# Performance work log

Hardware: AMD Instinct MI355X
Metric: run time of the kernel (lower is better)

Reference implementation:

```python
import jax, jax.numpy as jnp
import numpy as np

B, N, F, H, O = 8, 256, 128, 128, 64

def setup_inputs() -> dict:
    key = jax.random.key(0)
    ks = jax.random.split(key, 16)
    s = 0.02
    return {
        "local_x": jax.random.normal(ks[0], (B, N, F), jnp.float32),
        "global_x": jax.random.normal(ks[1], (B, N, F), jnp.float32),
        "mask": jax.random.uniform(ks[2], (B, N, N), jnp.float32),
        "key_idx": jax.random.randint(ks[3], (B,), 0, N),
        "hidden_state": jax.random.normal(ks[4], (B, N, H), jnp.float32),
        "fc_w": jax.random.normal(ks[5], (H, 3 * F), jnp.float32) * s,
        "fc_b": jnp.zeros((H,), jnp.float32),
        "ln_g": jnp.ones((H,), jnp.float32),
        "ln_b": jnp.zeros((H,), jnp.float32),
        "w_ih": jax.random.normal(ks[6], (3 * H, H), jnp.float32) * s,
        "w_hh": jax.random.normal(ks[7], (3 * H, H), jnp.float32) * s,
        "b_ih": jnp.zeros((3 * H,), jnp.float32),
        "b_hh": jnp.zeros((3 * H,), jnp.float32),
        "out_w": jax.random.normal(ks[8], (O, H), jnp.float32) * s,
        "out_b": jnp.zeros((O,), jnp.float32),
    }

def _forward(local_x, global_x, mask, key_idx, hidden_state,
             fc_w, fc_b, ln_g, ln_b, w_ih, w_hh, b_ih, b_hh, out_w, out_b):
    b, n, f = local_x.shape
    # masked mean aggregation over agents: same math as expand*mask then sum/den
    denom = mask.sum(axis=2, keepdims=True) + 1e-6            # [B,N,1]
    weak = jnp.einsum('bij,bjf->bif', mask, global_x) / denom  # [B,N,F]
    key_feat = jnp.take_along_axis(global_x, key_idx[:, None, None], axis=1)  # [B,1,F]
    key_feat = jnp.broadcast_to(key_feat, (b, n, f))
    combined = jnp.concatenate([local_x, weak, key_feat], axis=-1)  # [B,N,3F]
    h = combined @ fc_w.T + fc_b
    mu = h.mean(-1, keepdims=True)
    var = ((h - mu) ** 2).mean(-1, keepdims=True)
    h = (h - mu) / jnp.sqrt(var + 1e-5) * ln_g + ln_b
    x = jax.nn.relu(h)
    xf = x.reshape(-1, H)
    hf = hidden_state.reshape(-1, H)
    gi = xf @ w_ih.T + b_ih   # [BN,3H]
    gh = hf @ w_hh.T + b_hh
    i_r, i_z, i_n = jnp.split(gi, 3, axis=-1)
    h_r, h_z, h_n = jnp.split(gh, 3, axis=-1)
    r = jax.nn.sigmoid(i_r + h_r)
    z = jax.nn.sigmoid(i_z + h_z)
    nn_ = jnp.tanh(i_n + r * h_n)
    h_new = (1.0 - z) * nn_ + z * hf
    out = h_new @ out_w.T + out_b
    return out.reshape(b, n, -1), h_new.reshape(b, n, -1)

def reference(local_x, global_x, mask, key_idx, hidden_state,
              fc_w, fc_b, ln_g, ln_b, w_ih, w_hh, b_ih, b_hh, out_w, out_b):
    return _forward(local_x, global_x, mask, key_idx, hidden_state,
                    fc_w, fc_b, ln_g, ln_b, w_ih, w_hh, b_ih, b_hh, out_w, out_b)
```

## Files before the change

kernel.cpp:

```cpp
#include <hip/hip_runtime.h>

namespace {

typedef unsigned short ushort_t;
typedef unsigned int uint_t;
typedef __attribute__((ext_vector_type(8))) short short8v;
typedef __attribute__((ext_vector_type(4))) float f32x4;

constexpr int kB = 8, kN = 256, kF = 128, kH = 128, kO = 64;
constexpr int kR = 8;
constexpr int kTPB = 1024;
constexpr int kOut0 = kB * kN * kO;

constexpr int FW_WHH  = 0;
constexpr int FW_FCW  = 96;
constexpr int FW_WIH  = 192;
constexpr int FW_OUTW = 288;
constexpr int FW_GX   = 304;
constexpr int FW_TOTAL = 816;

union Frag {
    uint_t  u[4];
    short8v v;
};

__device__ __forceinline__ float waveReduceAdd(float v) {
    v += __shfl_xor(v, 1);
    v += __shfl_xor(v, 2);
    v += __shfl_xor(v, 4);
    v += __shfl_xor(v, 8);
    v += __shfl_xor(v, 16);
    v += __shfl_xor(v, 32);
    return v;
}

__device__ __forceinline__ ushort_t cvt1(float f) {
    return (ushort_t)((__float_as_uint(f) + 0x8000u) >> 16);
}
__device__ __forceinline__ uint_t pk(float f0, float f1) {
    uint_t b0 = __float_as_uint(f0) + 0x8000u;
    uint_t b1 = __float_as_uint(f1) + 0x8000u;
    return (b1 & 0xFFFF0000u) | (b0 >> 16);
}
__device__ __forceinline__ float b2f(ushort_t h) {
    return __uint_as_float(((uint_t)h) << 16);
}
__device__ __forceinline__ void loadWFrag(const float* __restrict__ p, Frag& b) {
    float4 lo = *(const float4*)p;
    float4 hi = *(const float4*)(p + 4);
    b.u[0] = pk(lo.x, lo.y);
    b.u[1] = pk(lo.z, lo.w);
    b.u[2] = pk(hi.x, hi.y);
    b.u[3] = pk(hi.z, hi.w);
}

__global__ __launch_bounds__(256) void convert_frags(
    const float* __restrict__ gx, const float* __restrict__ fc_w,
    const float* __restrict__ w_ih, const float* __restrict__ w_hh,
    const float* __restrict__ out_w, uint4* __restrict__ ws)
{
    const int gw = (int)((blockIdx.x * 256 + threadIdx.x) >> 6);
    if (gw >= FW_TOTAL) return;
    const int lane = threadIdx.x & 63;
    const int arow = lane & 15;
    const int kgrp = (lane >> 4) * 8;
    Frag fr;
    if (gw < FW_FCW) {
        int idx = gw - FW_WHH, t = idx >> 2, kf = idx & 3;
        loadWFrag(w_hh + (size_t)(t * 16 + arow) * kH + kf * 32 + kgrp, fr);
    } else if (gw < FW_WIH) {
        int idx = gw - FW_FCW, t = idx / 12, kf = idx % 12;
        loadWFrag(fc_w + (size_t)(t * 16 + arow) * 384 + kf * 32 + kgrp, fr);
    } else if (gw < FW_OUTW) {
        int idx = gw - FW_WIH, t = idx >> 2, kf = idx & 3;
        loadWFrag(w_ih + (size_t)(t * 16 + arow) * kH + kf * 32 + kgrp, fr);
    } else if (gw < FW_GX) {
        int idx = gw - FW_OUTW, t = idx >> 2, kf = idx & 3;
        loadWFrag(out_w + (size_t)(t * 16 + arow) * kH + kf * 32 + kgrp, fr);
    } else {
        int idx = gw - FW_GX;
        int bb = idx >> 6, rem = idx & 63, t = rem >> 3, kf = rem & 7;
        int k0 = kf * 32 + kgrp;
        const float* gp = gx + ((size_t)bb * kN + k0) * kF + t * 16 + arow;
        fr.u[0] = pk(gp[0 * kF], gp[1 * kF]);
        fr.u[1] = pk(gp[2 * kF], gp[3 * kF]);
        fr.u[2] = pk(gp[4 * kF], gp[5 * kF]);
        fr.u[3] = pk(gp[6 * kF], gp[7 * kF]);
    }
    ws[(size_t)gw * 64 + lane] = *(uint4*)fr.u;
}

__global__ __launch_bounds__(kTPB, 4) void weak_tie_fused(
    const float* __restrict__ lx, const float* __restrict__ gx,
    const float* __restrict__ mask, const int* __restrict__ key_idx,
    const float* __restrict__ hstate,
    const float* __restrict__ fc_b,
    const float* __restrict__ ln_g, const float* __restrict__ ln_b,
    const float* __restrict__ b_ih, const float* __restrict__ b_hh,
    const float* __restrict__ out_b,
    const uint4* __restrict__ ws,
    float* __restrict__ out)
{
    __shared__ __align__(16) ushort_t maskb[16][264];
    __shared__ __align__(16) ushort_t cmb[16][392];
    __shared__ __align__(16) ushort_t hf16[16][136];
    __shared__ __align__(16) ushort_t xb16[16][136];
    __shared__ __align__(16) ushort_t hnb16[16][136];
    __shared__ __align__(16) float hf32[kR * kH];
    __shared__ __align__(16) float hb[kR * kH];
    __shared__ __align__(16) ushort_t ghb[kR][384];
    __shared__ __align__(16) ushort_t gib[kR][384];
    __shared__ float denomInv[kR];

    const int tid  = threadIdx.x;
    const int b    = blockIdx.x >> 5;
    const int row0 = (blockIdx.x & 31) * kR;
    const int lane = tid & 63;
    const int wv   = tid >> 6;
    const int arow = lane & 15;
    const int kgrp = (lane >> 4) * 8;

    {
        const int r = tid >> 7, c = tid & 127;
        const float* mrow = mask + ((size_t)b * kN + row0) * kN;
        maskb[r][c]       = cvt1(mrow[r * 256 + c]);
        maskb[r][c + 128] = cvt1(mrow[r * 256 + c + 128]);
        const float* lrow = lx + ((size_t)b * kN + row0) * kF;
        cmb[r][c] = cvt1(lrow[tid]);
        const int ki = key_idx[b];
        cmb[r][256 + c] = cvt1(gx[((size_t)b * kN + ki) * kF + c]);
        const float* hrow = hstate + ((size_t)b * kN + row0) * kH;
        float hv = hrow[tid];
        hf32[tid] = hv;
        hf16[r][c] = cvt1(hv);
        uint_t* z;
        z = (uint_t*)&maskb[8][0]; for (int i = tid; i < 8 * 264 / 2; i += kTPB) z[i] = 0;
        z = (uint_t*)&cmb[8][0];   for (int i = tid; i < 8 * 392 / 2; i += kTPB) z[i] = 0;
        z = (uint_t*)&hf16[8][0];  for (int i = tid; i < 8 * 136 / 2; i += kTPB) z[i] = 0;
        z = (uint_t*)&xb16[8][0];  for (int i = tid; i < 8 * 136 / 2; i += kTPB) z[i] = 0;
        z = (uint_t*)&hnb16[8][0]; for (int i = tid; i < 8 * 136 / 2; i += kTPB) z[i] = 0;
    }
    __syncthreads();

    if (wv < 8) {
        int r = wv;
        float s = b2f(maskb[r][lane])       + b2f(maskb[r][lane + 64]) +
                  b2f(maskb[r][lane + 128]) + b2f(maskb[r][lane + 192]);
        s = waveReduceAdd(s);
        if (lane == 0) denomInv[r] = 1.0f / (s + 1e-6f);
    }
    __syncthreads();

    if (wv < 8) {
        const uint4* wsf = ws + ((size_t)(FW_GX + b * 64 + wv * 8) * 64 + lane);
        f32x4 acc = {0.f, 0.f, 0.f, 0.f};
        #pragma unroll
        for (int kf = 0; kf < 8; ++kf) {
            Frag a, bb;
            *(uint4*)a.u  = *(const uint4*)&maskb[arow][kf * 32 + kgrp];
            *(uint4*)bb.u = wsf[(size_t)kf * 64];
            acc = __builtin_amdgcn_mfma_f32_16x16x32_bf16(a.v, bb.v, acc, 0, 0, 0);
        }
        const int n0 = 16 * wv;
        #pragma unroll
        for (int j = 0; j < 4; ++j) {
            int row = (lane >> 4) * 4 + j;
            if (row < 8)
                cmb[row][128 + n0 + arow] = cvt1(acc[j] * denomInv[row]);
        }
    } else {
        const int w2 = wv - 8;
        Frag af[4];
        #pragma unroll
        for (int kf = 0; kf < 4; ++kf)
            *(uint4*)af[kf].u = *(const uint4*)&hf16[arow][kf * 32 + kgrp];
        #pragma unroll
        for (int t = 0; t < 3; ++t) {
            const int tile = w2 * 3 + t;
            const uint4* wsf = ws + ((size_t)(FW_WHH + tile * 4) * 64 + lane);
            f32x4 acc = {0.f, 0.f, 0.f, 0.f};
            #pragma unroll
            for (int kf = 0; kf < 4; ++kf) {
                Frag bb;
                *(uint4*)bb.u = wsf[(size_t)kf * 64];
                acc = __builtin_amdgcn_mfma_f32_16x16x32_bf16(af[kf].v, bb.v, acc, 0, 0, 0);
            }
            const int n0 = 16 * tile;
            #pragma unroll
            for (int j = 0; j < 4; ++j) {
                int row = (lane >> 4) * 4 + j;
                if (row < 8) ghb[row][n0 + arow] = cvt1(acc[j]);
            }
        }
    }
    __syncthreads();

    Frag bfr[12];
    if (wv < 8) {
        const uint4* wsf = ws + ((size_t)(FW_FCW + wv * 12) * 64 + lane);
        f32x4 acc = {0.f, 0.f, 0.f, 0.f};
        #pragma unroll
        for (int kf = 0; kf < 12; ++kf) {
            Frag a, bb;
            *(uint4*)a.u  = *(const uint4*)&cmb[arow][kf * 32 + kgrp];
            *(uint4*)bb.u = wsf[(size_t)kf * 64];
            acc = __builtin_amdgcn_mfma_f32_16x16x32_bf16(a.v, bb.v, acc, 0, 0, 0);
        }
        const int n0 = 16 * wv;
        #pragma unroll
        for (int j = 0; j < 4; ++j) {
            int row = (lane >> 4) * 4 + j;
            if (row < 8) hb[row * 128 + n0 + arow] = acc[j];
        }
    } else {
        const int w2 = wv - 8;
        #pragma unroll
        for (int t = 0; t < 3; ++t) {
            const int tile = w2 * 3 + t;
            const uint4* wsf = ws + ((size_t)(FW_WIH + tile * 4) * 64 + lane);
            #pragma unroll
            for (int kf = 0; kf < 4; ++kf)
                *(uint4*)bfr[t * 4 + kf].u = wsf[(size_t)kf * 64];
        }
    }
    __syncthreads();

    if (wv < 8) {
        int r = wv;
        float v0 = hb[r * 128 + lane]      + fc_b[lane];
        float v1 = hb[r * 128 + lane + 64] + fc_b[lane + 64];
        float s  = waveReduceAdd(v0 + v1);
        float ss = waveReduceAdd(v0 * v0 + v1 * v1);
        float mu   = s * (1.0f / 128.0f);
        float var  = ss * (1.0f / 128.0f) - mu * mu;
        float rstd = rsqrtf(var + 1e-5f);
        float x0 = fmaxf((v0 - mu) * rstd * ln_g[lane] + ln_b[lane], 0.f);
        float x1 = fmaxf((v1 - mu) * rstd * ln_g[lane + 64] + ln_b[lane + 64], 0.f);
        xb16[r][lane]      = cvt1(x0);
        xb16[r][lane + 64] = cvt1(x1);
    }
    __syncthreads();

    Frag obf[4];
    if (wv >= 8) {
        const int w2 = wv - 8;
        Frag af[4];
        #pragma unroll
        for (int kf = 0; kf < 4; ++kf)
            *(uint4*)af[kf].u = *(const uint4*)&xb16[arow][kf * 32 + kgrp];
        #pragma unroll
        for (int t = 0; t < 3; ++t) {
            const int n0 = 16 * (w2 * 3 + t);
            f32x4 acc = {0.f, 0.f, 0.f, 0.f};
            #pragma unroll
            for (int kf = 0; kf < 4; ++kf)
                acc = __builtin_amdgcn_mfma_f32_16x16x32_bf16(af[kf].v, bfr[t * 4 + kf].v, acc, 0, 0, 0);
            #pragma unroll
            for (int j = 0; j < 4; ++j) {
                int row = (lane >> 4) * 4 + j;
                if (row < 8) gib[row][n0 + arow] = cvt1(acc[j]);
            }
        }
    } else if (wv < 4) {
        const uint4* wsf = ws + ((size_t)(FW_OUTW + wv * 4) * 64 + lane);
        #pragma unroll
        for (int kf = 0; kf < 4; ++kf)
            *(uint4*)obf[kf].u = wsf[(size_t)kf * 64];
    }
    __syncthreads();

    {
        const int r = tid >> 7, fcol = tid & 127;
        float ir  = b2f(gib[r][fcol])       + b_ih[fcol];
        float iz  = b2f(gib[r][128 + fcol]) + b_ih[128 + fcol];
        float inn = b2f(gib[r][256 + fcol]) + b_ih[256 + fcol];
        float hr  = b2f(ghb[r][fcol])       + b_hh[fcol];
        float hz  = b2f(ghb[r][128 + fcol]) + b_hh[128 + fcol];
        float hn  = b2f(ghb[r][256 + fcol]) + b_hh[256 + fcol];
        float rg = 1.0f / (1.0f + __expf(-(ir + hr)));
        float zg = 1.0f / (1.0f + __expf(-(iz + hz)));
        float ng = tanhf(inn + rg * hn);
        float hprev = hf32[r * 128 + fcol];
        float hnew = (1.0f - zg) * ng + zg * hprev;
        hnb16[r][fcol] = cvt1(hnew);
        out[kOut0 + ((size_t)(b * kN + row0 + r)) * kH + fcol] = hnew;
    }
    __syncthreads();

    if (wv < 4) {
        const int n0 = 16 * wv;
        Frag af[4];
        #pragma unroll
        for (int kf = 0; kf < 4; ++kf)
            *(uint4*)af[kf].u = *(const uint4*)&hnb16[arow][kf * 32 + kgrp];
        f32x4 acc = {0.f, 0.f, 0.f, 0.f};
        #pragma unroll
        for (int kf = 0; kf < 4; ++kf)
            acc = __builtin_amdgcn_mfma_f32_16x16x32_bf16(af[kf].v, obf[kf].v, acc, 0, 0, 0);
        float ob = out_b[n0 + arow];
        #pragma unroll
        for (int j = 0; j < 4; ++j) {
            int row = (lane >> 4) * 4 + j;
            if (row < 8)
                out[((size_t)(b * kN + row0 + row)) * kO + n0 + arow] = acc[j] + ob;
        }
    }
}

}

extern "C" void kernel_launch(void* const* d_in, const int* in_sizes, int n_in,
                              void* d_out, int out_size, void* d_ws, size_t ws_size,
                              hipStream_t stream) {
    const float* lx      = (const float*)d_in[0];
    const float* gx      = (const float*)d_in[1];
    const float* mask    = (const float*)d_in[2];
    const int*   key_idx = (const int*)  d_in[3];
    const float* hs      = (const float*)d_in[4];
    const float* fc_w    = (const float*)d_in[5];
    const float* fc_b    = (const float*)d_in[6];
    const float* ln_g    = (const float*)d_in[7];
    const float* ln_b    = (const float*)d_in[8];
    const float* w_ih    = (const float*)d_in[9];
    const float* w_hh    = (const float*)d_in[10];
    const float* b_ih    = (const float*)d_in[11];
    const float* b_hh    = (const float*)d_in[12];
    const float* out_w   = (const float*)d_in[13];
    const float* out_b   = (const float*)d_in[14];
    float* out = (float*)d_out;
    uint4* ws = (uint4*)d_ws;

    hipLaunchKernelGGL(convert_frags, dim3((FW_TOTAL * 64) / 256), dim3(256), 0, stream,
                       gx, fc_w, w_ih, w_hh, out_w, ws);

    dim3 grid(kB * kN / kR);
    dim3 block(kTPB);
    hipLaunchKernelGGL(weak_tie_fused, grid, block, 0, stream,
                       lx, gx, mask, key_idx, hs,
                       fc_b, ln_g, ln_b,
                       b_ih, b_hh, out_b,
                       (const uint4*)ws, out);
}
```

Baseline: 19.32 us.

## Halve rows per block and rebalance waves across twice as many blocks

Each block now handles 4 node rows with 512 threads instead of 8 rows with 1024, doubling the grid to 512 blocks. The waves are reassigned: 4 waves each cover two output tiles of the aggregation and fc GEMMs, and 4 waves each cover six gate tiles. The zero-fill of the padding rows of the shared MFMA operand tiles is removed, since only rows 0-3 of each 16-row tile are written back. The aim is to spread the work over more CUs and shorten each block's serial critical path, at the cost of re-reading every weight fragment per block and wasting more of each 16-row MFMA tile.

```diff
diff --git a/kernel.cpp b/kernel.cpp
--- a/kernel.cpp
+++ b/kernel.cpp
@@ -8,8 +8,8 @@
 typedef __attribute__((ext_vector_type(4))) float f32x4;
 
 constexpr int kB = 8, kN = 256, kF = 128, kH = 128, kO = 64;
-constexpr int kR = 8;
-constexpr int kTPB = 1024;
+constexpr int kR = 4;
+constexpr int kTPB = 512;
 constexpr int kOut0 = kB * kN * kO;
 
 constexpr int FW_WHH  = 0;
@@ -113,8 +113,8 @@
     __shared__ float denomInv[kR];
 
     const int tid  = threadIdx.x;
-    const int b    = blockIdx.x >> 5;
-    const int row0 = (blockIdx.x & 31) * kR;
+    const int b    = blockIdx.x >> 6;
+    const int row0 = (blockIdx.x & 63) * kR;
     const int lane = tid & 63;
     const int wv   = tid >> 6;
     const int arow = lane & 15;
@@ -133,16 +133,10 @@
         float hv = hrow[tid];
         hf32[tid] = hv;
         hf16[r][c] = cvt1(hv);
-        uint_t* z;
-        z = (uint_t*)&maskb[8][0]; for (int i = tid; i < 8 * 264 / 2; i += kTPB) z[i] = 0;
-        z = (uint_t*)&cmb[8][0];   for (int i = tid; i < 8 * 392 / 2; i += kTPB) z[i] = 0;
-        z = (uint_t*)&hf16[8][0];  for (int i = tid; i < 8 * 136 / 2; i += kTPB) z[i] = 0;
-        z = (uint_t*)&xb16[8][0];  for (int i = tid; i < 8 * 136 / 2; i += kTPB) z[i] = 0;
-        z = (uint_t*)&hnb16[8][0]; for (int i = tid; i < 8 * 136 / 2; i += kTPB) z[i] = 0;
-    }
-    __syncthreads();
-
-    if (wv < 8) {
+    }
+    __syncthreads();
+
+    if (wv < kR) {
         int r = wv;
         float s = b2f(maskb[r][lane])       + b2f(maskb[r][lane + 64]) +
                   b2f(maskb[r][lane + 128]) + b2f(maskb[r][lane + 192]);
@@ -151,32 +145,37 @@
     }
     __syncthreads();
 
-    if (wv < 8) {
-        const uint4* wsf = ws + ((size_t)(FW_GX + b * 64 + wv * 8) * 64 + lane);
-        f32x4 acc = {0.f, 0.f, 0.f, 0.f};
-        #pragma unroll
-        for (int kf = 0; kf < 8; ++kf) {
-            Frag a, bb;
-            *(uint4*)a.u  = *(const uint4*)&maskb[arow][kf * 32 + kgrp];
-            *(uint4*)bb.u = wsf[(size_t)kf * 64];
-            acc = __builtin_amdgcn_mfma_f32_16x16x32_bf16(a.v, bb.v, acc, 0, 0, 0);
-        }
-        const int n0 = 16 * wv;
-        #pragma unroll
-        for (int j = 0; j < 4; ++j) {
-            int row = (lane >> 4) * 4 + j;
-            if (row < 8)
-                cmb[row][128 + n0 + arow] = cvt1(acc[j] * denomInv[row]);
+    if (wv < 4) {
+        Frag am[8];
+        #pragma unroll
+        for (int kf = 0; kf < 8; ++kf)
+            *(uint4*)am[kf].u = *(const uint4*)&maskb[arow][kf * 32 + kgrp];
+        #pragma unroll
+        for (int tt = 0; tt < 2; ++tt) {
+            const int t = wv * 2 + tt;
+            const uint4* wsf = ws + ((size_t)(FW_GX + b * 64 + t * 8) * 64 + lane);
+            f32x4 acc = {0.f, 0.f, 0.f, 0.f};
+            #pragma unroll
+            for (int kf = 0; kf < 8; ++kf) {
+                Frag bb;
+                *(uint4*)bb.u = wsf[(size_t)kf * 64];
+                acc = __builtin_amdgcn_mfma_f32_16x16x32_bf16(am[kf].v, bb.v, acc, 0, 0, 0);
+            }
+            const int n0 = 16 * t;
+            if ((lane >> 4) == 0) {
+                #pragma unroll
+                for (int j = 0; j < 4; ++j)
+                    cmb[j][128 + n0 + arow] = cvt1(acc[j] * denomInv[j]);
+            }
         }
     } else {
-        const int w2 = wv - 8;
         Frag af[4];
         #pragma unroll
         for (int kf = 0; kf < 4; ++kf)
             *(uint4*)af[kf].u = *(const uint4*)&hf16[arow][kf * 32 + kgrp];
         #pragma unroll
-        for (int t = 0; t < 3; ++t) {
-            const int tile = w2 * 3 + t;
+        for (int t6 = 0; t6 < 6; ++t6) {
+            const int tile = (wv - 4) * 6 + t6;
             const uint4* wsf = ws + ((size_t)(FW_WHH + tile * 4) * 64 + lane);
             f32x4 acc = {0.f, 0.f, 0.f, 0.f};
             #pragma unroll
@@ -186,46 +185,52 @@
                 acc = __builtin_amdgcn_mfma_f32_16x16x32_bf16(af[kf].v, bb.v, acc, 0, 0, 0);
             }
             const int n0 = 16 * tile;
-            #pragma unroll
-            for (int j = 0; j < 4; ++j) {
-                int row = (lane >> 4) * 4 + j;
-                if (row < 8) ghb[row][n0 + arow] = cvt1(acc[j]);
+            if ((lane >> 4) == 0) {
+                #pragma unroll
+                for (int j = 0; j < 4; ++j)
+                    ghb[j][n0 + arow] = cvt1(acc[j]);
             }
         }
     }
     __syncthreads();
 
     Frag bfr[12];
-    if (wv < 8) {
-        const uint4* wsf = ws + ((size_t)(FW_FCW + wv * 12) * 64 + lane);
-        f32x4 acc = {0.f, 0.f, 0.f, 0.f};
-        #pragma unroll
-        for (int kf = 0; kf < 12; ++kf) {
-            Frag a, bb;
-            *(uint4*)a.u  = *(const uint4*)&cmb[arow][kf * 32 + kgrp];
-            *(uint4*)bb.u = wsf[(size_t)kf * 64];
-            acc = __builtin_amdgcn_mfma_f32_16x16x32_bf16(a.v, bb.v, acc, 0, 0, 0);
-        }
-        const int n0 = 16 * wv;
-        #pragma unroll
-        for (int j = 0; j < 4; ++j) {
-            int row = (lane >> 4) * 4 + j;
-            if (row < 8) hb[row * 128 + n0 + arow] = acc[j];
+    if (wv < 4) {
+        Frag ac[12];
+        #pragma unroll
+        for (int kf = 0; kf < 12; ++kf)
+            *(uint4*)ac[kf].u = *(const uint4*)&cmb[arow][kf * 32 + kgrp];
+        #pragma unroll
+        for (int tt = 0; tt < 2; ++tt) {
+            const int t = wv * 2 + tt;
+            const uint4* wsf = ws + ((size_t)(FW_FCW + t * 12) * 64 + lane);
+            f32x4 acc = {0.f, 0.f, 0.f, 0.f};
+            #pragma unroll
+            for (int kf = 0; kf < 12; ++kf) {
+                Frag bb;
+                *(uint4*)bb.u = wsf[(size_t)kf * 64];
+                acc = __builtin_amdgcn_mfma_f32_16x16x32_bf16(ac[kf].v, bb.v, acc, 0, 0, 0);
+            }
+            const int n0 = 16 * t;
+            if ((lane >> 4) == 0) {
+                #pragma unroll
+                for (int j = 0; j < 4; ++j)
+                    hb[j * 128 + n0 + arow] = acc[j];
+            }
         }
     } else {
-        const int w2 = wv - 8;
-        #pragma unroll
-        for (int t = 0; t < 3; ++t) {
-            const int tile = w2 * 3 + t;
+        #pragma unroll
+        for (int t3 = 0; t3 < 3; ++t3) {
+            const int tile = (wv - 4) * 6 + t3;
             const uint4* wsf = ws + ((size_t)(FW_WIH + tile * 4) * 64 + lane);
             #pragma unroll
             for (int kf = 0; kf < 4; ++kf)
-                *(uint4*)bfr[t * 4 + kf].u = wsf[(size_t)kf * 64];
-        }
-    }
-    __syncthreads();
-
-    if (wv < 8) {
+                *(uint4*)bfr[t3 * 4 + kf].u = wsf[(size_t)kf * 64];
+        }
+    }
+    __syncthreads();
+
+    if (wv < kR) {
         int r = wv;
         float v0 = hb[r * 128 + lane]      + fc_b[lane];
         float v1 = hb[r * 128 + lane + 64] + fc_b[lane + 64];
@@ -242,26 +247,36 @@
     __syncthreads();
 
     Frag obf[4];
-    if (wv >= 8) {
-        const int w2 = wv - 8;
+    if (wv >= 4) {
         Frag af[4];
         #pragma unroll
         for (int kf = 0; kf < 4; ++kf)
             *(uint4*)af[kf].u = *(const uint4*)&xb16[arow][kf * 32 + kgrp];
         #pragma unroll
-        for (int t = 0; t < 3; ++t) {
-            const int n0 = 16 * (w2 * 3 + t);
+        for (int t6 = 0; t6 < 6; ++t6) {
+            const int tile = (wv - 4) * 6 + t6;
             f32x4 acc = {0.f, 0.f, 0.f, 0.f};
-            #pragma unroll
-            for (int kf = 0; kf < 4; ++kf)
-                acc = __builtin_amdgcn_mfma_f32_16x16x32_bf16(af[kf].v, bfr[t * 4 + kf].v, acc, 0, 0, 0);
-            #pragma unroll
-            for (int j = 0; j < 4; ++j) {
-                int row = (lane >> 4) * 4 + j;
-                if (row < 8) gib[row][n0 + arow] = cvt1(acc[j]);
-            }
-        }
-    } else if (wv < 4) {
+            if (t6 < 3) {
+                #pragma unroll
+                for (int kf = 0; kf < 4; ++kf)
+                    acc = __builtin_amdgcn_mfma_f32_16x16x32_bf16(af[kf].v, bfr[t6 * 4 + kf].v, acc, 0, 0, 0);
+            } else {
+                const uint4* wsf = ws + ((size_t)(FW_WIH + tile * 4) * 64 + lane);
+                #pragma unroll
+                for (int kf = 0; kf < 4; ++kf) {
+                    Frag bb;
+                    *(uint4*)bb.u = wsf[(size_t)kf * 64];
+                    acc = __builtin_amdgcn_mfma_f32_16x16x32_bf16(af[kf].v, bb.v, acc, 0, 0, 0);
+                }
+            }
+            const int n0 = 16 * tile;
+            if ((lane >> 4) == 0) {
+                #pragma unroll
+                for (int j = 0; j < 4; ++j)
+                    gib[j][n0 + arow] = cvt1(acc[j]);
+            }
+        }
+    } else {
         const uint4* wsf = ws + ((size_t)(FW_OUTW + wv * 4) * 64 + lane);
         #pragma unroll
         for (int kf = 0; kf < 4; ++kf)
@@ -297,12 +312,11 @@
         #pragma unroll
         for (int kf = 0; kf < 4; ++kf)
             acc = __builtin_amdgcn_mfma_f32_16x16x32_bf16(af[kf].v, obf[kf].v, acc, 0, 0, 0);
-        float ob = out_b[n0 + arow];
-        #pragma unroll
-        for (int j = 0; j < 4; ++j) {
-            int row = (lane >> 4) * 4 + j;
-            if (row < 8)
-                out[((size_t)(b * kN + row0 + row)) * kO + n0 + arow] = acc[j] + ob;
+        if ((lane >> 4) == 0) {
+            float ob = out_b[n0 + arow];
+            #pragma unroll
+            for (int j = 0; j < 4; ++j)
+                out[((size_t)(b * kN + row0 + j)) * kO + n0 + arow] = acc[j] + ob;
         }
     }
 }
```

Result: slower. 22.18 us (+14.8%).

## Fuse GRU gate epilogue into MFMA waves and drop shared-memory gate buffers

Applied to the files above, without the earlier changes.

The W_hh and W_ih tiles are remapped so each wave computes the r, z and n gate tiles for the same 16 hidden columns. The GRU nonlinearity then runs directly on accumulator registers, which removes the ghb/gib shared buffers, a barrier and a separate elementwise phase. The mask row sum now reads global memory in the load phase, which removes another barrier. The global_x and fc_w weight fragments are prefetched earlier, zeroing of the padding rows is dropped, and sigmoid and tanh use fast reciprocal/exp forms. The risks are higher register pressure from the prefetched fragments and slightly different numerics, since gates now stay in fp32 instead of rounding to bf16 and use fast approximations.

```diff
diff --git a/kernel.cpp b/kernel.cpp
--- a/kernel.cpp
+++ b/kernel.cpp
@@ -42,8 +42,13 @@
     uint_t b1 = __float_as_uint(f1) + 0x8000u;
     return (b1 & 0xFFFF0000u) | (b0 >> 16);
 }
-__device__ __forceinline__ float b2f(ushort_t h) {
-    return __uint_as_float(((uint_t)h) << 16);
+__device__ __forceinline__ float sigm(float x) {
+    return __builtin_amdgcn_rcpf(1.0f + __expf(-x));
+}
+__device__ __forceinline__ float tanh_fast(float x) {
+    x = fminf(fmaxf(x, -15.0f), 15.0f);
+    float e = __expf(2.0f * x);
+    return (e - 1.0f) * __builtin_amdgcn_rcpf(e + 1.0f);
 }
 __device__ __forceinline__ void loadWFrag(const float* __restrict__ p, Frag& b) {
     float4 lo = *(const float4*)p;
@@ -90,6 +95,8 @@
     ws[(size_t)gw * 64 + lane] = *(uint4*)fr.u;
 }
 
+#define MFMA16(A, B, C) __builtin_amdgcn_mfma_f32_16x16x32_bf16((A), (B), (C), 0, 0, 0)
+
 __global__ __launch_bounds__(kTPB, 4) void weak_tie_fused(
     const float* __restrict__ lx, const float* __restrict__ gx,
     const float* __restrict__ mask, const int* __restrict__ key_idx,
@@ -108,8 +115,6 @@
     __shared__ __align__(16) ushort_t hnb16[16][136];
     __shared__ __align__(16) float hf32[kR * kH];
     __shared__ __align__(16) float hb[kR * kH];
-    __shared__ __align__(16) ushort_t ghb[kR][384];
-    __shared__ __align__(16) ushort_t gib[kR][384];
     __shared__ float denomInv[kR];
 
     const int tid  = threadIdx.x;
@@ -120,53 +125,52 @@
     const int arow = lane & 15;
     const int kgrp = (lane >> 4) * 8;
 
+    Frag wkf[8];
+    if (wv < 8) {
+        const uint4* wsf = ws + ((size_t)(FW_GX + b * 64 + wv * 8) * 64 + lane);
+        #pragma unroll
+        for (int kf = 0; kf < 8; ++kf) *(uint4*)wkf[kf].u = wsf[(size_t)kf * 64];
+    }
     {
         const int r = tid >> 7, c = tid & 127;
         const float* mrow = mask + ((size_t)b * kN + row0) * kN;
         maskb[r][c]       = cvt1(mrow[r * 256 + c]);
         maskb[r][c + 128] = cvt1(mrow[r * 256 + c + 128]);
-        const float* lrow = lx + ((size_t)b * kN + row0) * kF;
-        cmb[r][c] = cvt1(lrow[tid]);
+        cmb[r][c] = cvt1(lx[((size_t)b * kN + row0) * kF + tid]);
         const int ki = key_idx[b];
         cmb[r][256 + c] = cvt1(gx[((size_t)b * kN + ki) * kF + c]);
-        const float* hrow = hstate + ((size_t)b * kN + row0) * kH;
-        float hv = hrow[tid];
+        float hv = hstate[((size_t)b * kN + row0) * kH + tid];
         hf32[tid] = hv;
         hf16[r][c] = cvt1(hv);
-        uint_t* z;
-        z = (uint_t*)&maskb[8][0]; for (int i = tid; i < 8 * 264 / 2; i += kTPB) z[i] = 0;
-        z = (uint_t*)&cmb[8][0];   for (int i = tid; i < 8 * 392 / 2; i += kTPB) z[i] = 0;
-        z = (uint_t*)&hf16[8][0];  for (int i = tid; i < 8 * 136 / 2; i += kTPB) z[i] = 0;
-        z = (uint_t*)&xb16[8][0];  for (int i = tid; i < 8 * 136 / 2; i += kTPB) z[i] = 0;
-        z = (uint_t*)&hnb16[8][0]; for (int i = tid; i < 8 * 136 / 2; i += kTPB) z[i] = 0;
-    }
-    __syncthreads();
-
-    if (wv < 8) {
-        int r = wv;
-        float s = b2f(maskb[r][lane])       + b2f(maskb[r][lane + 64]) +
-                  b2f(maskb[r][lane + 128]) + b2f(maskb[r][lane + 192]);
-        s = waveReduceAdd(s);
-        if (lane == 0) denomInv[r] = 1.0f / (s + 1e-6f);
-    }
-    __syncthreads();
-
-    if (wv < 8) {
-        const uint4* wsf = ws + ((size_t)(FW_GX + b * 64 + wv * 8) * 64 + lane);
+    }
+    if (wv < 8) {
+        const float* mr = mask + ((size_t)b * kN + row0 + wv) * kN;
+        float4 m4 = *(const float4*)(mr + lane * 4);
+        float s = waveReduceAdd(m4.x + m4.y + m4.z + m4.w);
+        if (lane == 0) denomInv[wv] = 1.0f / (s + 1e-6f);
+    }
+    __syncthreads();
+
+    f32x4 gh0 = {0.f, 0.f, 0.f, 0.f}, gh1 = gh0, gh2 = gh0;
+    Frag fcf[12];
+    if (wv < 8) {
         f32x4 acc = {0.f, 0.f, 0.f, 0.f};
         #pragma unroll
         for (int kf = 0; kf < 8; ++kf) {
-            Frag a, bb;
-            *(uint4*)a.u  = *(const uint4*)&maskb[arow][kf * 32 + kgrp];
-            *(uint4*)bb.u = wsf[(size_t)kf * 64];
-            acc = __builtin_amdgcn_mfma_f32_16x16x32_bf16(a.v, bb.v, acc, 0, 0, 0);
-        }
+            Frag a;
+            *(uint4*)a.u = *(const uint4*)&maskb[arow][kf * 32 + kgrp];
+            acc = MFMA16(a.v, wkf[kf].v, acc);
+        }
+        const uint4* wsf = ws + ((size_t)(FW_FCW + wv * 12) * 64 + lane);
+        #pragma unroll
+        for (int kf = 0; kf < 12; ++kf) *(uint4*)fcf[kf].u = wsf[(size_t)kf * 64];
         const int n0 = 16 * wv;
-        #pragma unroll
-        for (int j = 0; j < 4; ++j) {
-            int row = (lane >> 4) * 4 + j;
-            if (row < 8)
+        if (lane < 32) {
+            #pragma unroll
+            for (int j = 0; j < 4; ++j) {
+                int row = (lane >> 4) * 4 + j;
                 cmb[row][128 + n0 + arow] = cvt1(acc[j] * denomInv[row]);
+            }
         }
     } else {
         const int w2 = wv - 8;
@@ -174,53 +178,49 @@
         #pragma unroll
         for (int kf = 0; kf < 4; ++kf)
             *(uint4*)af[kf].u = *(const uint4*)&hf16[arow][kf * 32 + kgrp];
-        #pragma unroll
-        for (int t = 0; t < 3; ++t) {
-            const int tile = w2 * 3 + t;
-            const uint4* wsf = ws + ((size_t)(FW_WHH + tile * 4) * 64 + lane);
-            f32x4 acc = {0.f, 0.f, 0.f, 0.f};
-            #pragma unroll
-            for (int kf = 0; kf < 4; ++kf) {
-                Frag bb;
-                *(uint4*)bb.u = wsf[(size_t)kf * 64];
-                acc = __builtin_amdgcn_mfma_f32_16x16x32_bf16(af[kf].v, bb.v, acc, 0, 0, 0);
-            }
-            const int n0 = 16 * tile;
+        const uint4* p0 = ws + ((size_t)(FW_WHH + w2 * 4) * 64 + lane);
+        const uint4* p1 = ws + ((size_t)(FW_WHH + (8 + w2) * 4) * 64 + lane);
+        const uint4* p2 = ws + ((size_t)(FW_WHH + (16 + w2) * 4) * 64 + lane);
+        #pragma unroll
+        for (int kf = 0; kf < 4; ++kf) {
+            Frag b0, b1, b2;
+            *(uint4*)b0.u = p0[(size_t)kf * 64];
+            *(uint4*)b1.u = p1[(size_t)kf * 64];
+            *(uint4*)b2.u = p2[(size_t)kf * 64];
+            gh0 = MFMA16(af[kf].v, b0.v, gh0);
+            gh1 = MFMA16(af[kf].v, b1.v, gh1);
+            gh2 = MFMA16(af[kf].v, b2.v, gh2);
+        }
+    }
+    __syncthreads();
+
+    Frag bfr[12];
+    if (wv < 8) {
+        f32x4 acc = {0.f, 0.f, 0.f, 0.f};
+        #pragma unroll
+        for (int kf = 0; kf < 12; ++kf) {
+            Frag a;
+            *(uint4*)a.u = *(const uint4*)&cmb[arow][kf * 32 + kgrp];
+            acc = MFMA16(a.v, fcf[kf].v, acc);
+        }
+        const int n0 = 16 * wv;
+        if (lane < 32) {
             #pragma unroll
             for (int j = 0; j < 4; ++j) {
                 int row = (lane >> 4) * 4 + j;
-                if (row < 8) ghb[row][n0 + arow] = cvt1(acc[j]);
+                hb[row * 128 + n0 + arow] = acc[j];
             }
-        }
-    }
-    __syncthreads();
-
-    Frag bfr[12];
-    if (wv < 8) {
-        const uint4* wsf = ws + ((size_t)(FW_FCW + wv * 12) * 64 + lane);
-        f32x4 acc = {0.f, 0.f, 0.f, 0.f};
-        #pragma unroll
-        for (int kf = 0; kf < 12; ++kf) {
-            Frag a, bb;
-            *(uint4*)a.u  = *(const uint4*)&cmb[arow][kf * 32 + kgrp];
-            *(uint4*)bb.u = wsf[(size_t)kf * 64];
-            acc = __builtin_amdgcn_mfma_f32_16x16x32_bf16(a.v, bb.v, acc, 0, 0, 0);
-        }
-        const int n0 = 16 * wv;
-        #pragma unroll
-        for (int j = 0; j < 4; ++j) {
-            int row = (lane >> 4) * 4 + j;
-            if (row < 8) hb[row * 128 + n0 + arow] = acc[j];
         }
     } else {
         const int w2 = wv - 8;
-        #pragma unroll
-        for (int t = 0; t < 3; ++t) {
-            const int tile = w2 * 3 + t;
-            const uint4* wsf = ws + ((size_t)(FW_WIH + tile * 4) * 64 + lane);
-            #pragma unroll
-            for (int kf = 0; kf < 4; ++kf)
-                *(uint4*)bfr[t * 4 + kf].u = wsf[(size_t)kf * 64];
+        const uint4* p0 = ws + ((size_t)(FW_WIH + w2 * 4) * 64 + lane);
+        const uint4* p1 = ws + ((size_t)(FW_WIH + (8 + w2) * 4) * 64 + lane);
+        const uint4* p2 = ws + ((size_t)(FW_WIH + (16 + w2) * 4) * 64 + lane);
+        #pragma unroll
+        for (int kf = 0; kf < 4; ++kf) {
+            *(uint4*)bfr[kf].u     = p0[(size_t)kf * 64];
+            *(uint4*)bfr[4 + kf].u = p1[(size_t)kf * 64];
+            *(uint4*)bfr[8 + kf].u = p2[(size_t)kf * 64];
         }
     }
     __syncthreads();
@@ -248,17 +248,27 @@
         #pragma unroll
         for (int kf = 0; kf < 4; ++kf)
             *(uint4*)af[kf].u = *(const uint4*)&xb16[arow][kf * 32 + kgrp];
-        #pragma unroll
-        for (int t = 0; t < 3; ++t) {
-            const int n0 = 16 * (w2 * 3 + t);
-            f32x4 acc = {0.f, 0.f, 0.f, 0.f};
-            #pragma unroll
-            for (int kf = 0; kf < 4; ++kf)
-                acc = __builtin_amdgcn_mfma_f32_16x16x32_bf16(af[kf].v, bfr[t * 4 + kf].v, acc, 0, 0, 0);
+        f32x4 gi0 = {0.f, 0.f, 0.f, 0.f}, gi1 = gi0, gi2 = gi0;
+        #pragma unroll
+        for (int kf = 0; kf < 4; ++kf) {
+            gi0 = MFMA16(af[kf].v, bfr[kf].v, gi0);
+            gi1 = MFMA16(af[kf].v, bfr[4 + kf].v, gi1);
+            gi2 = MFMA16(af[kf].v, bfr[8 + kf].v, gi2);
+        }
+        if (lane < 32) {
+            const int f = w2 * 16 + arow;
+            float bir = b_ih[f], biz = b_ih[128 + f], bin = b_ih[256 + f];
+            float bhr = b_hh[f], bhz = b_hh[128 + f], bhn = b_hh[256 + f];
             #pragma unroll
             for (int j = 0; j < 4; ++j) {
                 int row = (lane >> 4) * 4 + j;
-                if (row < 8) gib[row][n0 + arow] = cvt1(acc[j]);
+                float rg = sigm(gi0[j] + bir + gh0[j] + bhr);
+                float zg = sigm(gi1[j] + biz + gh1[j] + bhz);
+                float ng = tanh_fast(gi2[j] + bin + rg * (gh2[j] + bhn));
+                float hprev = hf32[row * 128 + f];
+                float hnew = (1.0f - zg) * ng + zg * hprev;
+                hnb16[row][f] = cvt1(hnew);
+                out[kOut0 + ((size_t)(b * kN + row0 + row)) * kH + f] = hnew;
             }
         }
     } else if (wv < 4) {
@@ -269,40 +279,22 @@
     }
     __syncthreads();
 
-    {
-        const int r = tid >> 7, fcol = tid & 127;
-        float ir  = b2f(gib[r][fcol])       + b_ih[fcol];
-        float iz  = b2f(gib[r][128 + fcol]) + b_ih[128 + fcol];
-        float inn = b2f(gib[r][256 + fcol]) + b_ih[256 + fcol];
-        float hr  = b2f(ghb[r][fcol])       + b_hh[fcol];
-        float hz  = b2f(ghb[r][128 + fcol]) + b_hh[128 + fcol];
-        float hn  = b2f(ghb[r][256 + fcol]) + b_hh[256 + fcol];
-        float rg = 1.0f / (1.0f + __expf(-(ir + hr)));
-        float zg = 1.0f / (1.0f + __expf(-(iz + hz)));
-        float ng = tanhf(inn + rg * hn);
-        float hprev = hf32[r * 128 + fcol];
-        float hnew = (1.0f - zg) * ng + zg * hprev;
-        hnb16[r][fcol] = cvt1(hnew);
-        out[kOut0 + ((size_t)(b * kN + row0 + r)) * kH + fcol] = hnew;
-    }
-    __syncthreads();
-
     if (wv < 4) {
         const int n0 = 16 * wv;
-        Frag af[4];
-        #pragma unroll
-        for (int kf = 0; kf < 4; ++kf)
-            *(uint4*)af[kf].u = *(const uint4*)&hnb16[arow][kf * 32 + kgrp];
         f32x4 acc = {0.f, 0.f, 0.f, 0.f};
         #pragma unroll
-        for (int kf = 0; kf < 4; ++kf)
-            acc = __builtin_amdgcn_mfma_f32_16x16x32_bf16(af[kf].v, obf[kf].v, acc, 0, 0, 0);
-        float ob = out_b[n0 + arow];
-        #pragma unroll
-        for (int j = 0; j < 4; ++j) {
-            int row = (lane >> 4) * 4 + j;
-            if (row < 8)
+        for (int kf = 0; kf < 4; ++kf) {
+            Frag a;
+            *(uint4*)a.u = *(const uint4*)&hnb16[arow][kf * 32 + kgrp];
+            acc = MFMA16(a.v, obf[kf].v, acc);
+        }
+        if (lane < 32) {
+            float ob = out_b[n0 + arow];
+            #pragma unroll
+            for (int j = 0; j < 4; ++j) {
+                int row = (lane >> 4) * 4 + j;
                 out[((size_t)(b * kN + row0 + row)) * kO + n0 + arow] = acc[j] + ob;
+            }
         }
     }
 }
```

Result: faster. 18.43 us (-4.6%).
